# Performance work log

Measured on AMD Instinct MI355X. Metric: run time of the kernel, lower is better.

Reference implementation:

```python
import jax, jax.numpy as jnp
import numpy as np

N = 50000      # nodes
E = 800000     # edges (avg degree 16)
G = 50         # graphs in batch (1000 nodes each)
D_IN, H, H2, OUT = 8, 128, 64, 1


def setup_inputs() -> dict:
    key = jax.random.key(0)
    ks = jax.random.split(key, 16)
    src = jax.random.randint(ks[0], (E,), 0, N)
    # every node gets at least one in-edge (forward computes 3/in_deg)
    dst = jnp.concatenate([jnp.arange(N), jax.random.randint(ks[1], (E - N,), 0, N)])
    graph_ids = jnp.arange(N) // (N // G)

    def lin(k, fan_in, fan_out):
        return jax.random.normal(k, (fan_in, fan_out), jnp.float32) / np.float32(np.sqrt(fan_in))

    inp = {"src": src, "dst": dst, "graph_ids": graph_ids}
    dims = [(D_IN, H), (H, H), (H, H), (H, H), (H, H)]
    for i, (fi, fo) in enumerate(dims):
        inp[f"W{i+1}"] = lin(ks[2 + i], fi, fo)
        inp[f"b{i+1}"] = jnp.zeros((fo,), jnp.float32)
    inp["lw1"] = lin(ks[8], H, H2)
    inp["lb1"] = jnp.zeros((H2,), jnp.float32)
    inp["lw2"] = lin(ks[9], H2, OUT)
    inp["lb2"] = jnp.zeros((OUT,), jnp.float32)
    return inp


def reference(src, dst, graph_ids, W1, b1, W2, b2, W3, b3, W4, b4, W5, b5, lw1, lb1, lw2, lb2):
    ones_e = jnp.ones((E,), jnp.float32)
    in_deg = jax.ops.segment_sum(ones_e, dst, num_segments=N)   # [N]
    out_deg = jax.ops.segment_sum(ones_e, src, num_segments=N)  # [N]

    # degree features (8 channels)
    h1 = in_deg[:, None]
    h2 = (in_deg > 3.0).astype(jnp.float32)[:, None]
    h3 = 3.0 / h1
    h4 = (in_deg > 4.0).astype(jnp.float32)[:, None]
    h_ = jnp.concatenate([h1, h2, h3, h4, -h1, -h2, -h3, -h4], axis=1)  # [N,8]

    # DGL GraphConv norm='both': clamp degrees to min 1 for normalization
    norm_src = jnp.maximum(out_deg, 1.0) ** -0.5  # [N]
    norm_dst = jnp.maximum(in_deg, 1.0) ** -0.5   # [N]

    def conv(h, W, b):
        m = (h * norm_src[:, None])[src]                        # [E, d] gather
        agg = jax.ops.segment_sum(m, dst, num_segments=N)       # [N, d] scatter-add
        return agg * norm_dst[:, None] @ W + b

    h_co = jax.nn.relu(conv(h_, W1, b1))
    h_co = jax.nn.relu(conv(h_co, W2, b2))
    h_co = jax.nn.relu(conv(h_co, W3, b3))
    h_co = jax.nn.relu(conv(h_co, W4, b4))
    h_co = jax.nn.relu(conv(h_co, W5, b5))                      # [N, H]

    # dgl.mean_nodes: per-graph mean pool
    counts = jax.ops.segment_sum(jnp.ones((N,), jnp.float32), graph_ids, num_segments=G)
    graph_emb = jax.ops.segment_sum(h_co, graph_ids, num_segments=G) / counts[:, None]  # [G, H]

    # dropout layers are identity in eval mode
    h_emb = jax.nn.relu(graph_emb @ lw1 + lb1)
    pred = jax.nn.sigmoid(h_emb @ lw2 + lb2)                    # [G, 1]
    return (pred, graph_emb, h_co)
```

## Files before the change

kernel.cpp:

```cpp
#include <hip/hip_runtime.h>
#include <math.h>

#define N_NODES 50000
#define N_EDGES 800000
#define N_GRAPHS 50
#define HD 128
#define TM 64
#define LDA 68
#define POOL_CHUNK 125
#define SCAN_B 256
#define SCAN_NB ((N_NODES + SCAN_B - 1) / SCAN_B)
#define NB_H 128
#define CH_H (N_EDGES / NB_H)
#define NBIN2 (N_NODES / 2)

__global__ __launch_bounds__(256) void k_hist(const int* __restrict__ src,
                                              const int* __restrict__ dst,
                                              unsigned* __restrict__ part_in,
                                              unsigned* __restrict__ part_out) {
    __shared__ unsigned cnt[NBIN2];
    int t = threadIdx.x, b = blockIdx.x;
    int e0 = b * CH_H;
    for (int j = t; j < NBIN2; j += 256) cnt[j] = 0;
    __syncthreads();
    for (int e = e0 + t; e < e0 + CH_H; e += 256) {
        int i = dst[e];
        atomicAdd(&cnt[i >> 1], 1u << ((i & 1) * 16));
    }
    __syncthreads();
    for (int j = t; j < NBIN2; j += 256) part_in[b * NBIN2 + j] = cnt[j];
    __syncthreads();
    for (int j = t; j < NBIN2; j += 256) cnt[j] = 0;
    __syncthreads();
    for (int e = e0 + t; e < e0 + CH_H; e += 256) {
        int i = src[e];
        atomicAdd(&cnt[i >> 1], 1u << ((i & 1) * 16));
    }
    __syncthreads();
    for (int j = t; j < NBIN2; j += 256) part_out[b * NBIN2 + j] = cnt[j];
}

__global__ void k_dreduce(unsigned* __restrict__ part_in,
                          const unsigned* __restrict__ part_out,
                          int* __restrict__ deg_in, int* __restrict__ deg_out) {
    int j = blockIdx.x * blockDim.x + threadIdx.x;
    if (j >= NBIN2) return;
    unsigned run_i = 0, run_o = 0;
    for (int b = 0; b < NB_H; ++b) {
        unsigned pi = part_in[b * NBIN2 + j];
        unsigned po = part_out[b * NBIN2 + j];
        part_in[b * NBIN2 + j] = run_i;
        run_i += pi;
        run_o += po;
    }
    ((int2*)deg_in)[j] = make_int2((int)(run_i & 0xFFFFu), (int)(run_i >> 16));
    ((int2*)deg_out)[j] = make_int2((int)(run_o & 0xFFFFu), (int)(run_o >> 16));
}

__global__ void k_norms(const int* __restrict__ deg_in, const int* __restrict__ deg_out,
                        const int* __restrict__ gids,
                        float* norm_src, float* norm_dst, int* gcount,
                        float4* __restrict__ feat4) {
    __shared__ int hist[N_GRAPHS];
    int t = threadIdx.x;
    if (t < N_GRAPHS) hist[t] = 0;
    __syncthreads();
    int i = blockIdx.x * blockDim.x + t;
    if (i < N_NODES) {
        float di = (float)deg_in[i];
        float dq = (float)deg_out[i];
        float nd = 1.0f / sqrtf(fmaxf(di, 1.0f));
        float ns = 1.0f / sqrtf(fmaxf(dq, 1.0f));
        norm_dst[i] = nd;
        norm_src[i] = ns;
        float4 f;
        f.x = di * ns;
        f.y = (di > 3.0f) ? ns : 0.0f;
        f.z = (3.0f / di) * ns;
        f.w = (di > 4.0f) ? ns : 0.0f;
        feat4[i] = f;
        atomicAdd(&hist[gids[i]], 1);
    }
    __syncthreads();
    if (t < N_GRAPHS && hist[t] != 0) atomicAdd(&gcount[t], hist[t]);
}

__global__ void k_scan1(const int* __restrict__ deg_in, int* off, int* bsum) {
    __shared__ int sh[SCAN_B];
    int t = threadIdx.x;
    int i = blockIdx.x * SCAN_B + t;
    int v = (i < N_NODES) ? deg_in[i] : 0;
    sh[t] = v;
    __syncthreads();
    for (int o = 1; o < SCAN_B; o <<= 1) {
        int u = (t >= o) ? sh[t - o] : 0;
        __syncthreads();
        sh[t] += u;
        __syncthreads();
    }
    if (i < N_NODES) off[i] = sh[t] - v;
    if (t == SCAN_B - 1) bsum[blockIdx.x] = sh[t];
}

__global__ void k_scan2(int* bsum, int* off) {
    __shared__ int sh[SCAN_B];
    int t = threadIdx.x;
    int v = (t < SCAN_NB) ? bsum[t] : 0;
    sh[t] = v;
    __syncthreads();
    for (int o = 1; o < SCAN_B; o <<= 1) {
        int u = (t >= o) ? sh[t - o] : 0;
        __syncthreads();
        sh[t] += u;
        __syncthreads();
    }
    if (t < SCAN_NB) bsum[t] = sh[t] - v;
    if (t == SCAN_B - 1) off[N_NODES] = sh[t];
}

__global__ void k_scan3(int* off, const int* __restrict__ bsum) {
    int b = blockIdx.x, t = threadIdx.x;
    int i = b * SCAN_B + t;
    if (i < N_NODES) off[i] += bsum[b];
}

__global__ __launch_bounds__(256) void k_scatter2(const int* __restrict__ src,
                                                  const int* __restrict__ dst,
                                                  const int* __restrict__ off,
                                                  const unsigned* __restrict__ part_in,
                                                  int* __restrict__ csr) {
    __shared__ unsigned cur[NBIN2];
    int t = threadIdx.x, b = blockIdx.x;
    const unsigned* base = part_in + (size_t)b * NBIN2;
    for (int j = t; j < NBIN2; j += 256) cur[j] = base[j];
    __syncthreads();
    int e0 = b * CH_H;
    for (int e = e0 + t; e < e0 + CH_H; e += 256) {
        int d = dst[e];
        int sh = (d & 1) * 16;
        unsigned old = atomicAdd(&cur[d >> 1], 1u << sh);
        int rank = (int)((old >> sh) & 0xFFFFu);
        csr[off[d] + rank] = src[e];
    }
}

__global__ void k_agg1(const int* __restrict__ off, const int* __restrict__ csr,
                       const float4* __restrict__ feat4,
                       const float* __restrict__ ndst, float* __restrict__ agg8) {
    int i = blockIdx.x * blockDim.x + threadIdx.x;
    if (i >= N_NODES) return;
    int e0 = off[i], e1 = off[i + 1];
    float a0 = 0.f, a1 = 0.f, a2 = 0.f, a3 = 0.f;
    int e = e0;
    for (; e + 1 < e1; e += 2) {
        float4 f0 = feat4[csr[e]];
        float4 f1 = feat4[csr[e + 1]];
        a0 += f0.x + f1.x; a1 += f0.y + f1.y;
        a2 += f0.z + f1.z; a3 += f0.w + f1.w;
    }
    if (e < e1) {
        float4 f0 = feat4[csr[e]];
        a0 += f0.x; a1 += f0.y; a2 += f0.z; a3 += f0.w;
    }
    float nd = ndst[i];
    a0 *= nd; a1 *= nd; a2 *= nd; a3 *= nd;
    float4* p = (float4*)(agg8 + (size_t)i * 8);
    float4 hi = { a0, a1, a2, a3 };
    float4 lo = { -a0, -a1, -a2, -a3 };
    p[0] = hi;
    p[1] = lo;
}

__global__ void k_gemm1(const float* __restrict__ agg8, const float* __restrict__ W,
                        const float* __restrict__ b, const float* __restrict__ nsrc,
                        float* __restrict__ out) {
    __shared__ float Wsh[8 * 128];
    int t = threadIdx.x;
    for (int i = t; i < 1024; i += 256) Wsh[i] = W[i];
    __syncthreads();
    int row = blockIdx.x * 2 + (t >> 7);
    int j = t & 127;
    if (row >= N_NODES) return;
    const float* a = agg8 + (size_t)row * 8;
    float acc = b[j];
#pragma unroll
    for (int k = 0; k < 8; ++k) acc += a[k] * Wsh[k * 128 + j];
    out[(size_t)row * HD + j] = fmaxf(acc, 0.0f) * nsrc[row];
}

__global__ __launch_bounds__(256) void k_agg4(const int* __restrict__ off,
                                              const int* __restrict__ csr,
                                              const float* __restrict__ ndst,
                                              const float* __restrict__ h,
                                              float* __restrict__ out) {
    int wid = (blockIdx.x * blockDim.x + threadIdx.x) >> 6;
    int lane = threadIdx.x & 63;
    if (wid >= N_NODES) return;
    int half = lane >> 5;
    int q = lane & 31;
    int e0 = off[wid], e1 = off[wid + 1];
    float4 a = { 0.f, 0.f, 0.f, 0.f };
    int e = e0 + half;
    for (; e + 6 < e1; e += 8) {
        int s0 = csr[e], s1 = csr[e + 2], s2 = csr[e + 4], s3 = csr[e + 6];
        float4 v0 = *(const float4*)(h + (size_t)s0 * HD + q * 4);
        float4 v1 = *(const float4*)(h + (size_t)s1 * HD + q * 4);
        float4 v2 = *(const float4*)(h + (size_t)s2 * HD + q * 4);
        float4 v3 = *(const float4*)(h + (size_t)s3 * HD + q * 4);
        a.x += v0.x + v1.x + v2.x + v3.x;
        a.y += v0.y + v1.y + v2.y + v3.y;
        a.z += v0.z + v1.z + v2.z + v3.z;
        a.w += v0.w + v1.w + v2.w + v3.w;
    }
    for (; e < e1; e += 2) {
        int s0 = csr[e];
        float4 v0 = *(const float4*)(h + (size_t)s0 * HD + q * 4);
        a.x += v0.x; a.y += v0.y; a.z += v0.z; a.w += v0.w;
    }
    a.x += __shfl_xor(a.x, 32);
    a.y += __shfl_xor(a.y, 32);
    a.z += __shfl_xor(a.z, 32);
    a.w += __shfl_xor(a.w, 32);
    if (half == 0) {
        float nd = ndst[wid];
        a.x *= nd; a.y *= nd; a.z *= nd; a.w *= nd;
        *(float4*)(out + (size_t)wid * HD + q * 4) = a;
    }
}

__global__ void k_agg2(const int* __restrict__ off, const int* __restrict__ csr,
                       const float* __restrict__ ndst,
                       const float* __restrict__ h, float* __restrict__ out) {
    int wid = (blockIdx.x * blockDim.x + threadIdx.x) >> 6;
    int lane = threadIdx.x & 63;
    if (wid >= N_NODES) return;
    int e0 = off[wid], e1 = off[wid + 1];
    float a0 = 0.f, a1 = 0.f;
    int e = e0;
    for (; e + 3 < e1; e += 4) {
        int s0 = csr[e], s1 = csr[e + 1], s2 = csr[e + 2], s3 = csr[e + 3];
        float2 v0 = *(const float2*)(h + (size_t)s0 * HD + lane * 2);
        float2 v1 = *(const float2*)(h + (size_t)s1 * HD + lane * 2);
        float2 v2 = *(const float2*)(h + (size_t)s2 * HD + lane * 2);
        float2 v3 = *(const float2*)(h + (size_t)s3 * HD + lane * 2);
        a0 += v0.x + v1.x + v2.x + v3.x;
        a1 += v0.y + v1.y + v2.y + v3.y;
    }
    for (; e < e1; ++e) {
        int s0 = csr[e];
        float2 v0 = *(const float2*)(h + (size_t)s0 * HD + lane * 2);
        a0 += v0.x; a1 += v0.y;
    }
    float nd = ndst[wid];
    float2 o; o.x = a0 * nd; o.y = a1 * nd;
    *(float2*)(out + (size_t)wid * HD + lane * 2) = o;
}

__global__ __launch_bounds__(512) void k_gemm(const float* __restrict__ A,
                                              const float* __restrict__ W,
                                              const float* __restrict__ b,
                                              const float* __restrict__ nsrc,
                                              int premult,
                                              float* __restrict__ out) {
    __shared__ float Wsh[128 * 128];
    __shared__ float Ash[128 * LDA];
    int t = threadIdx.x;
    const float4* W4 = (const float4*)W;
    float4* Wsh4 = (float4*)Wsh;
#pragma unroll
    for (int i = 0; i < 8; ++i) Wsh4[t + i * 512] = W4[t + i * 512];
    int row0 = blockIdx.x * TM;
#pragma unroll
    for (int i = 0; i < 4; ++i) {
        int idx = t + i * 512;
        int r = idx >> 5;
        int q = idx & 31;
        int row = row0 + r;
        if (row >= N_NODES) row = N_NODES - 1;
        float4 v = ((const float4*)(A + (size_t)row * HD))[q];
        Ash[(4 * q + 0) * LDA + r] = v.x;
        Ash[(4 * q + 1) * LDA + r] = v.y;
        Ash[(4 * q + 2) * LDA + r] = v.z;
        Ash[(4 * q + 3) * LDA + r] = v.w;
    }
    __syncthreads();
    int j0 = (t & 31) * 4;
    int r0 = (t >> 5) * 4;
    float4 bv = *(const float4*)(b + j0);
    float acc[4][4];
#pragma unroll
    for (int r = 0; r < 4; ++r) {
        acc[r][0] = bv.x; acc[r][1] = bv.y; acc[r][2] = bv.z; acc[r][3] = bv.w;
    }
#pragma unroll 4
    for (int k = 0; k < 128; ++k) {
        float4 w = *(const float4*)&Wsh[k * 128 + j0];
        float4 a = *(const float4*)&Ash[k * LDA + r0];
        acc[0][0] += a.x * w.x; acc[0][1] += a.x * w.y; acc[0][2] += a.x * w.z; acc[0][3] += a.x * w.w;
        acc[1][0] += a.y * w.x; acc[1][1] += a.y * w.y; acc[1][2] += a.y * w.z; acc[1][3] += a.y * w.w;
        acc[2][0] += a.z * w.x; acc[2][1] += a.z * w.y; acc[2][2] += a.z * w.z; acc[2][3] += a.z * w.w;
        acc[3][0] += a.w * w.x; acc[3][1] += a.w * w.y; acc[3][2] += a.w * w.z; acc[3][3] += a.w * w.w;
    }
#pragma unroll
    for (int r = 0; r < 4; ++r) {
        int row = row0 + r0 + r;
        if (row < N_NODES) {
            float sc = premult ? nsrc[row] : 1.0f;
            float* op = out + (size_t)row * HD + j0;
            float2 o01 = { fmaxf(acc[r][0], 0.f) * sc, fmaxf(acc[r][1], 0.f) * sc };
            float2 o23 = { fmaxf(acc[r][2], 0.f) * sc, fmaxf(acc[r][3], 0.f) * sc };
            *(float2*)op = o01;
            *(float2*)(op + 2) = o23;
        }
    }
}

__global__ void k_pool(const float* __restrict__ hco, const int* __restrict__ gids,
                       float* gsum) {
    int f = threadIdx.x;
    int n0 = blockIdx.x * POOL_CHUNK;
    int g = gids[n0];
    float s = 0.f;
    for (int i = 0; i < POOL_CHUNK; ++i)
        s += hco[(size_t)(n0 + i) * HD + f];
    atomicAdd(&gsum[g * HD + f], s);
}

__global__ void k_head(const float* __restrict__ gsum, const int* __restrict__ gcount,
                       const float* __restrict__ lw1, const float* __restrict__ lb1,
                       const float* __restrict__ lw2, const float* __restrict__ lb2,
                       float* __restrict__ dout) {
    __shared__ float ge[128];
    int g = blockIdx.x, j = threadIdx.x;
    float cnt = (float)gcount[g];
    float g0 = gsum[g * HD + j] / cnt;
    float g1 = gsum[g * HD + 64 + j] / cnt;
    ge[j] = g0; ge[64 + j] = g1;
    dout[N_GRAPHS + g * HD + j] = g0;
    dout[N_GRAPHS + g * HD + 64 + j] = g1;
    __syncthreads();
    float acc = lb1[j];
#pragma unroll 4
    for (int k = 0; k < 128; ++k) acc += ge[k] * lw1[k * 64 + j];
    float he = fmaxf(acc, 0.f);
    float p = he * lw2[j];
#pragma unroll
    for (int o = 32; o > 0; o >>= 1) p += __shfl_down(p, o);
    if (j == 0) dout[g] = 1.0f / (1.0f + expf(-(p + lb2[0])));
}

extern "C" void kernel_launch(void* const* d_in, const int* in_sizes, int n_in,
                              void* d_out, int out_size, void* d_ws, size_t ws_size,
                              hipStream_t stream) {
    const int* src  = (const int*)d_in[0];
    const int* dst  = (const int*)d_in[1];
    const int* gids = (const int*)d_in[2];
    const float* W1 = (const float*)d_in[3];  const float* b1 = (const float*)d_in[4];
    const float* W2 = (const float*)d_in[5];  const float* b2 = (const float*)d_in[6];
    const float* W3 = (const float*)d_in[7];  const float* b3 = (const float*)d_in[8];
    const float* W4 = (const float*)d_in[9];  const float* b4 = (const float*)d_in[10];
    const float* W5 = (const float*)d_in[11]; const float* b5 = (const float*)d_in[12];
    const float* lw1 = (const float*)d_in[13]; const float* lb1 = (const float*)d_in[14];
    const float* lw2 = (const float*)d_in[15]; const float* lb2 = (const float*)d_in[16];
    float* out = (float*)d_out;

    char* ws = (char*)d_ws;
    int*    gcount   = (int*)(ws + 0);
    float*  gsum     = (float*)(ws + 256);
    const size_t ZERO_BYTES = 25856;
    int*    deg_in   = (int*)(ws + 26112);
    int*    deg_out  = (int*)(ws + 226304);
    int*    off      = (int*)(ws + 426496);
    int*    csr      = (int*)(ws + 826880);
    float*  norm_src = (float*)(ws + 4026880);
    float*  norm_dst = (float*)(ws + 4227072);
    int*    bsum     = (int*)(ws + 4427264);
    float4* feat4    = (float4*)(ws + 4428288);
    float*  aggbuf   = (float*)(ws + 5228544);
    float*  hws      = (float*)(ws + 30828544);
    const size_t WS_NEEDED = 30828544 + 25600000;

    unsigned* part_in  = (unsigned*)aggbuf;
    unsigned* part_out = (unsigned*)aggbuf + NB_H * NBIN2;

    float* hco = out + (N_GRAPHS + N_GRAPHS * HD);
    bool aligned = (ws_size >= WS_NEEDED);
    float* hbuf = aligned ? hws : hco;

    hipMemsetAsync(ws, 0, ZERO_BYTES, stream);

    k_hist<<<NB_H, 256, 0, stream>>>(src, dst, part_in, part_out);
    k_dreduce<<<(NBIN2 + 255) / 256, 256, 0, stream>>>(part_in, part_out,
                                                       deg_in, deg_out);
    k_norms<<<(N_NODES + 255) / 256, 256, 0, stream>>>(deg_in, deg_out, gids,
                                                       norm_src, norm_dst, gcount, feat4);
    k_scan1<<<SCAN_NB, SCAN_B, 0, stream>>>(deg_in, off, bsum);
    k_scan2<<<1, SCAN_B, 0, stream>>>(bsum, off);
    k_scan3<<<SCAN_NB, SCAN_B, 0, stream>>>(off, bsum);
    k_scatter2<<<NB_H, 256, 0, stream>>>(src, dst, off, part_in, csr);

    k_agg1<<<(N_NODES + 255) / 256, 256, 0, stream>>>(off, csr, feat4, norm_dst, aggbuf);
    k_gemm1<<<N_NODES / 2, 256, 0, stream>>>(aggbuf, W1, b1, norm_src, hbuf);

    const float* Ws[4] = { W2, W3, W4, W5 };
    const float* bs[4] = { b2, b3, b4, b5 };
    for (int L = 0; L < 4; ++L) {
        if (aligned)
            k_agg4<<<(N_NODES * 64 + 255) / 256, 256, 0, stream>>>(off, csr,
                                                                   norm_dst, hbuf, aggbuf);
        else
            k_agg2<<<(N_NODES * 64 + 255) / 256, 256, 0, stream>>>(off, csr,
                                                                   norm_dst, hbuf, aggbuf);
        float* gout = (L < 3) ? hbuf : hco;
        k_gemm<<<(N_NODES + TM - 1) / TM, 512, 0, stream>>>(aggbuf, Ws[L], bs[L],
                                                            norm_src, (L < 3) ? 1 : 0,
                                                            gout);
    }

    k_pool<<<N_NODES / POOL_CHUNK, 128, 0, stream>>>(hco, gids, gsum);
    k_head<<<N_GRAPHS, 64, 0, stream>>>(gsum, gcount, lw1, lb1, lw2, lb2, out);
}
```

Measured before the change: 519.7 us.

## Store hidden features in 16-column strips and retile the dense GEMM

Hidden features are written in a column-strip layout (8 strips of 16 floats per node), so each aggregation pass gathers 64-byte rows from a 3.2MB strip that fits in cache. This is meant to cut the random-gather DRAM traffic of the 128-wide aggregation. The GEMM moves from 64-row tiles with 4x4 per-thread blocks to 128-row tiles with 8x8 per-thread blocks and a padded, swizzled shared layout. The larger tiles need more LDS and registers per thread, which may lower occupancy, and the aggregation kernel now runs 8 times as many blocks.

```diff
diff --git a/kernel.cpp b/kernel.cpp
--- a/kernel.cpp
+++ b/kernel.cpp
@@ -5,14 +5,20 @@
 #define N_EDGES 800000
 #define N_GRAPHS 50
 #define HD 128
-#define TM 64
-#define LDA 68
 #define POOL_CHUNK 125
 #define SCAN_B 256
 #define SCAN_NB ((N_NODES + SCAN_B - 1) / SCAN_B)
 #define NB_H 128
 #define CH_H (N_EDGES / NB_H)
 #define NBIN2 (N_NODES / 2)
+#define NPASS 8
+#define STRIP 16
+#define NPBLK (N_NODES / 4)
+#define GLDA 140
+
+__device__ __forceinline__ int sidx(int k, int c) {
+    return k * GLDA + c + ((c >> 5) << 2);
+}
 
 __global__ __launch_bounds__(256) void k_hist(const int* __restrict__ src,
                                               const int* __restrict__ dst,
@@ -173,7 +179,7 @@
 
 __global__ void k_gemm1(const float* __restrict__ agg8, const float* __restrict__ W,
                         const float* __restrict__ b, const float* __restrict__ nsrc,
-                        float* __restrict__ out) {
+                        int blocked, float* __restrict__ out) {
     __shared__ float Wsh[8 * 128];
     int t = threadIdx.x;
     for (int i = t; i < 1024; i += 256) Wsh[i] = W[i];
@@ -185,46 +191,42 @@
     float acc = b[j];
 #pragma unroll
     for (int k = 0; k < 8; ++k) acc += a[k] * Wsh[k * 128 + j];
-    out[(size_t)row * HD + j] = fmaxf(acc, 0.0f) * nsrc[row];
-}
-
-__global__ __launch_bounds__(256) void k_agg4(const int* __restrict__ off,
+    float v = fmaxf(acc, 0.0f) * nsrc[row];
+    if (blocked)
+        out[((size_t)(j >> 4) * N_NODES + row) * STRIP + (j & 15)] = v;
+    else
+        out[(size_t)row * HD + j] = v;
+}
+
+__global__ __launch_bounds__(256) void k_aggp(const int* __restrict__ off,
                                               const int* __restrict__ csr,
                                               const float* __restrict__ ndst,
                                               const float* __restrict__ h,
-                                              float* __restrict__ out) {
-    int wid = (blockIdx.x * blockDim.x + threadIdx.x) >> 6;
+                                              float* __restrict__ agg) {
+    int bx = blockIdx.x;
+    int pass = bx / NPBLK;
+    int node = (bx - pass * NPBLK) * 4 + (threadIdx.x >> 6);
     int lane = threadIdx.x & 63;
-    if (wid >= N_NODES) return;
-    int half = lane >> 5;
-    int q = lane & 31;
-    int e0 = off[wid], e1 = off[wid + 1];
+    int slot = lane >> 2, q = lane & 3;
+    const float* hp = h + (size_t)pass * N_NODES * STRIP;
+    int e0 = off[node], e1 = off[node + 1];
     float4 a = { 0.f, 0.f, 0.f, 0.f };
-    int e = e0 + half;
-    for (; e + 6 < e1; e += 8) {
-        int s0 = csr[e], s1 = csr[e + 2], s2 = csr[e + 4], s3 = csr[e + 6];
-        float4 v0 = *(const float4*)(h + (size_t)s0 * HD + q * 4);
-        float4 v1 = *(const float4*)(h + (size_t)s1 * HD + q * 4);
-        float4 v2 = *(const float4*)(h + (size_t)s2 * HD + q * 4);
-        float4 v3 = *(const float4*)(h + (size_t)s3 * HD + q * 4);
-        a.x += v0.x + v1.x + v2.x + v3.x;
-        a.y += v0.y + v1.y + v2.y + v3.y;
-        a.z += v0.z + v1.z + v2.z + v3.z;
-        a.w += v0.w + v1.w + v2.w + v3.w;
-    }
-    for (; e < e1; e += 2) {
-        int s0 = csr[e];
-        float4 v0 = *(const float4*)(h + (size_t)s0 * HD + q * 4);
-        a.x += v0.x; a.y += v0.y; a.z += v0.z; a.w += v0.w;
-    }
-    a.x += __shfl_xor(a.x, 32);
-    a.y += __shfl_xor(a.y, 32);
-    a.z += __shfl_xor(a.z, 32);
-    a.w += __shfl_xor(a.w, 32);
-    if (half == 0) {
-        float nd = ndst[wid];
-        a.x *= nd; a.y *= nd; a.z *= nd; a.w *= nd;
-        *(float4*)(out + (size_t)wid * HD + q * 4) = a;
+    for (int e = e0 + slot; e < e1; e += 16) {
+        int s = csr[e];
+        float4 v = *(const float4*)(hp + (size_t)s * STRIP + q * 4);
+        a.x += v.x; a.y += v.y; a.z += v.z; a.w += v.w;
+    }
+#pragma unroll
+    for (int m = 4; m <= 32; m <<= 1) {
+        a.x += __shfl_xor(a.x, m);
+        a.y += __shfl_xor(a.y, m);
+        a.z += __shfl_xor(a.z, m);
+        a.w += __shfl_xor(a.w, m);
+    }
+    if (lane < 4) {
+        float nd = ndst[node];
+        float4 o = { a.x * nd, a.y * nd, a.z * nd, a.w * nd };
+        *(float4*)(agg + (size_t)node * HD + pass * STRIP + lane * 4) = o;
     }
 }
 
@@ -256,61 +258,88 @@
     *(float2*)(out + (size_t)wid * HD + lane * 2) = o;
 }
 
-__global__ __launch_bounds__(512) void k_gemm(const float* __restrict__ A,
+__global__ __launch_bounds__(256) void k_gemm(const float* __restrict__ A,
                                               const float* __restrict__ W,
                                               const float* __restrict__ b,
                                               const float* __restrict__ nsrc,
-                                              int premult,
+                                              int mode,
                                               float* __restrict__ out) {
-    __shared__ float Wsh[128 * 128];
-    __shared__ float Ash[128 * LDA];
+    __shared__ float Wsh[128 * GLDA];
+    __shared__ float Ash[128 * GLDA];
     int t = threadIdx.x;
-    const float4* W4 = (const float4*)W;
-    float4* Wsh4 = (float4*)Wsh;
-#pragma unroll
-    for (int i = 0; i < 8; ++i) Wsh4[t + i * 512] = W4[t + i * 512];
-    int row0 = blockIdx.x * TM;
-#pragma unroll
-    for (int i = 0; i < 4; ++i) {
-        int idx = t + i * 512;
-        int r = idx >> 5;
-        int q = idx & 31;
-        int row = row0 + r;
-        if (row >= N_NODES) row = N_NODES - 1;
-        float4 v = ((const float4*)(A + (size_t)row * HD))[q];
-        Ash[(4 * q + 0) * LDA + r] = v.x;
-        Ash[(4 * q + 1) * LDA + r] = v.y;
-        Ash[(4 * q + 2) * LDA + r] = v.z;
-        Ash[(4 * q + 3) * LDA + r] = v.w;
-    }
-    __syncthreads();
-    int j0 = (t & 31) * 4;
-    int r0 = (t >> 5) * 4;
-    float4 bv = *(const float4*)(b + j0);
-    float acc[4][4];
-#pragma unroll
-    for (int r = 0; r < 4; ++r) {
-        acc[r][0] = bv.x; acc[r][1] = bv.y; acc[r][2] = bv.z; acc[r][3] = bv.w;
-    }
-#pragma unroll 4
+    int row0 = blockIdx.x * 128;
+    {
+        const float4* W4 = (const float4*)W;
+#pragma unroll
+        for (int i = 0; i < 16; ++i) {
+            int idx = t + i * 256;
+            int k = idx >> 5;
+            int q = idx & 31;
+            float4 v = W4[idx];
+            Wsh[sidx(k, 4 * q + 0)] = v.x;
+            Wsh[sidx(k, 4 * q + 1)] = v.y;
+            Wsh[sidx(k, 4 * q + 2)] = v.z;
+            Wsh[sidx(k, 4 * q + 3)] = v.w;
+        }
+        const float4* A4 = (const float4*)A;
+#pragma unroll
+        for (int i = 0; i < 16; ++i) {
+            int idx = t + i * 256;
+            int q = idx >> 7;
+            int r = idx & 127;
+            int row = row0 + r;
+            if (row >= N_NODES) row = N_NODES - 1;
+            float4 v = A4[(size_t)row * 32 + q];
+            Ash[sidx(4 * q + 0, r)] = v.x;
+            Ash[sidx(4 * q + 1, r)] = v.y;
+            Ash[sidx(4 * q + 2, r)] = v.z;
+            Ash[sidx(4 * q + 3, r)] = v.w;
+        }
+    }
+    __syncthreads();
+    int tx = t & 15, ty = t >> 4;
+    int j0 = tx * 8, r0 = ty * 8;
+    float acc[8][8];
+#pragma unroll
+    for (int c = 0; c < 8; ++c) {
+        float bc = b[j0 + c];
+#pragma unroll
+        for (int r = 0; r < 8; ++r) acc[r][c] = bc;
+    }
+#pragma unroll 2
     for (int k = 0; k < 128; ++k) {
-        float4 w = *(const float4*)&Wsh[k * 128 + j0];
-        float4 a = *(const float4*)&Ash[k * LDA + r0];
-        acc[0][0] += a.x * w.x; acc[0][1] += a.x * w.y; acc[0][2] += a.x * w.z; acc[0][3] += a.x * w.w;
-        acc[1][0] += a.y * w.x; acc[1][1] += a.y * w.y; acc[1][2] += a.y * w.z; acc[1][3] += a.y * w.w;
-        acc[2][0] += a.z * w.x; acc[2][1] += a.z * w.y; acc[2][2] += a.z * w.z; acc[2][3] += a.z * w.w;
-        acc[3][0] += a.w * w.x; acc[3][1] += a.w * w.y; acc[3][2] += a.w * w.z; acc[3][3] += a.w * w.w;
-    }
-#pragma unroll
-    for (int r = 0; r < 4; ++r) {
+        float4 w0 = *(const float4*)&Wsh[sidx(k, j0)];
+        float4 w1 = *(const float4*)&Wsh[sidx(k, j0 + 4)];
+        float4 a0 = *(const float4*)&Ash[sidx(k, r0)];
+        float4 a1 = *(const float4*)&Ash[sidx(k, r0 + 4)];
+        float wv[8] = { w0.x, w0.y, w0.z, w0.w, w1.x, w1.y, w1.z, w1.w };
+        float av[8] = { a0.x, a0.y, a0.z, a0.w, a1.x, a1.y, a1.z, a1.w };
+#pragma unroll
+        for (int r = 0; r < 8; ++r)
+#pragma unroll
+            for (int c = 0; c < 8; ++c) acc[r][c] += av[r] * wv[c];
+    }
+#pragma unroll
+    for (int r = 0; r < 8; ++r) {
         int row = row0 + r0 + r;
-        if (row < N_NODES) {
-            float sc = premult ? nsrc[row] : 1.0f;
+        if (row >= N_NODES) continue;
+        if (mode == 0) {
+            float sc = nsrc[row];
+            float* op = out + ((size_t)(j0 >> 4) * N_NODES + row) * STRIP + (j0 & 15);
+            float4 o0 = { fmaxf(acc[r][0], 0.f) * sc, fmaxf(acc[r][1], 0.f) * sc,
+                          fmaxf(acc[r][2], 0.f) * sc, fmaxf(acc[r][3], 0.f) * sc };
+            float4 o1 = { fmaxf(acc[r][4], 0.f) * sc, fmaxf(acc[r][5], 0.f) * sc,
+                          fmaxf(acc[r][6], 0.f) * sc, fmaxf(acc[r][7], 0.f) * sc };
+            *(float4*)op = o0;
+            *(float4*)(op + 4) = o1;
+        } else {
+            float sc = (mode == 1) ? nsrc[row] : 1.0f;
             float* op = out + (size_t)row * HD + j0;
-            float2 o01 = { fmaxf(acc[r][0], 0.f) * sc, fmaxf(acc[r][1], 0.f) * sc };
-            float2 o23 = { fmaxf(acc[r][2], 0.f) * sc, fmaxf(acc[r][3], 0.f) * sc };
-            *(float2*)op = o01;
-            *(float2*)(op + 2) = o23;
+#pragma unroll
+            for (int c = 0; c < 8; c += 2) {
+                float2 o = { fmaxf(acc[r][c], 0.f) * sc, fmaxf(acc[r][c + 1], 0.f) * sc };
+                *(float2*)(op + c) = o;
+            }
         }
     }
 }
@@ -385,7 +414,6 @@
 
     float* hco = out + (N_GRAPHS + N_GRAPHS * HD);
     bool aligned = (ws_size >= WS_NEEDED);
-    float* hbuf = aligned ? hws : hco;
 
     hipMemsetAsync(ws, 0, ZERO_BYTES, stream);
 
@@ -400,21 +428,22 @@
     k_scatter2<<<NB_H, 256, 0, stream>>>(src, dst, off, part_in, csr);
 
     k_agg1<<<(N_NODES + 255) / 256, 256, 0, stream>>>(off, csr, feat4, norm_dst, aggbuf);
-    k_gemm1<<<N_NODES / 2, 256, 0, stream>>>(aggbuf, W1, b1, norm_src, hbuf);
+    float* hbuf = aligned ? hws : hco;
+    k_gemm1<<<N_NODES / 2, 256, 0, stream>>>(aggbuf, W1, b1, norm_src,
+                                             aligned ? 1 : 0, hbuf);
 
     const float* Ws[4] = { W2, W3, W4, W5 };
     const float* bs[4] = { b2, b3, b4, b5 };
     for (int L = 0; L < 4; ++L) {
         if (aligned)
-            k_agg4<<<(N_NODES * 64 + 255) / 256, 256, 0, stream>>>(off, csr,
-                                                                   norm_dst, hbuf, aggbuf);
+            k_aggp<<<NPASS * NPBLK, 256, 0, stream>>>(off, csr, norm_dst, hws, aggbuf);
         else
             k_agg2<<<(N_NODES * 64 + 255) / 256, 256, 0, stream>>>(off, csr,
-                                                                   norm_dst, hbuf, aggbuf);
+                                                                   norm_dst, hco, aggbuf);
+        int mode = (L < 3) ? (aligned ? 0 : 1) : 2;
         float* gout = (L < 3) ? hbuf : hco;
-        k_gemm<<<(N_NODES + TM - 1) / TM, 512, 0, stream>>>(aggbuf, Ws[L], bs[L],
-                                                            norm_src, (L < 3) ? 1 : 0,
-                                                            gout);
+        k_gemm<<<(N_NODES + 127) / 128, 256, 0, stream>>>(aggbuf, Ws[L], bs[L],
+                                                          norm_src, mode, gout);
     }
 
     k_pool<<<N_NODES / POOL_CHUNK, 128, 0, stream>>>(hco, gids, gsum);
```

After: 769.1 us. 1.48x slower.

## Fuse neighbor aggregation into GEMM kernel for hidden GCN layers

Applied to the files above, without the earlier changes.

Replaces the separate aggregation and GEMM launches of layers 2-5 with one kernel. Each 512-thread block gathers and sums neighbor features for its 64 nodes straight into shared memory, then multiplies by the weight tile held in shared memory. Layer outputs ping-pong between two buffers. This removes the round trip of the aggregated matrix through global memory and half the launches. In exchange, each block now runs a serial gather of 8 nodes per wavefront before its GEMM, with heavy shared-memory use limiting occupancy, so latency hiding in the gather may get worse. The fallback GEMM load is also split into two float2 loads, apparently for alignment.

```diff
diff --git a/kernel.cpp b/kernel.cpp
--- a/kernel.cpp
+++ b/kernel.cpp
@@ -188,43 +188,91 @@
     out[(size_t)row * HD + j] = fmaxf(acc, 0.0f) * nsrc[row];
 }
 
-__global__ __launch_bounds__(256) void k_agg4(const int* __restrict__ off,
-                                              const int* __restrict__ csr,
-                                              const float* __restrict__ ndst,
-                                              const float* __restrict__ h,
-                                              float* __restrict__ out) {
-    int wid = (blockIdx.x * blockDim.x + threadIdx.x) >> 6;
-    int lane = threadIdx.x & 63;
-    if (wid >= N_NODES) return;
-    int half = lane >> 5;
-    int q = lane & 31;
-    int e0 = off[wid], e1 = off[wid + 1];
-    float4 a = { 0.f, 0.f, 0.f, 0.f };
-    int e = e0 + half;
-    for (; e + 6 < e1; e += 8) {
-        int s0 = csr[e], s1 = csr[e + 2], s2 = csr[e + 4], s3 = csr[e + 6];
-        float4 v0 = *(const float4*)(h + (size_t)s0 * HD + q * 4);
-        float4 v1 = *(const float4*)(h + (size_t)s1 * HD + q * 4);
-        float4 v2 = *(const float4*)(h + (size_t)s2 * HD + q * 4);
-        float4 v3 = *(const float4*)(h + (size_t)s3 * HD + q * 4);
-        a.x += v0.x + v1.x + v2.x + v3.x;
-        a.y += v0.y + v1.y + v2.y + v3.y;
-        a.z += v0.z + v1.z + v2.z + v3.z;
-        a.w += v0.w + v1.w + v2.w + v3.w;
-    }
-    for (; e < e1; e += 2) {
-        int s0 = csr[e];
-        float4 v0 = *(const float4*)(h + (size_t)s0 * HD + q * 4);
-        a.x += v0.x; a.y += v0.y; a.z += v0.z; a.w += v0.w;
-    }
-    a.x += __shfl_xor(a.x, 32);
-    a.y += __shfl_xor(a.y, 32);
-    a.z += __shfl_xor(a.z, 32);
-    a.w += __shfl_xor(a.w, 32);
-    if (half == 0) {
-        float nd = ndst[wid];
-        a.x *= nd; a.y *= nd; a.z *= nd; a.w *= nd;
-        *(float4*)(out + (size_t)wid * HD + q * 4) = a;
+__global__ __launch_bounds__(512) void k_aggemm(const int* __restrict__ off,
+                                                const int* __restrict__ csr,
+                                                const float* __restrict__ ndst,
+                                                const float* __restrict__ h,
+                                                const float* __restrict__ W,
+                                                const float* __restrict__ b,
+                                                const float* __restrict__ nsrc,
+                                                int premult,
+                                                float* __restrict__ out) {
+    __shared__ float Wsh[128 * 128];
+    __shared__ float Ash[128 * LDA];
+    int t = threadIdx.x;
+    const float4* W4 = (const float4*)W;
+    float4* Wsh4 = (float4*)Wsh;
+#pragma unroll
+    for (int i = 0; i < 8; ++i) Wsh4[t + i * 512] = W4[t + i * 512];
+
+    int row0 = blockIdx.x * TM;
+    int w = t >> 6, lane = t & 63;
+    int half = lane >> 5, q = lane & 31;
+    for (int i = 0; i < 8; ++i) {
+        int r = w * 8 + i;
+        int node = row0 + r;
+        if (node >= N_NODES) break;
+        int e0 = off[node], e1 = off[node + 1];
+        float4 a = { 0.f, 0.f, 0.f, 0.f };
+        int e = e0 + half;
+        for (; e + 6 < e1; e += 8) {
+            int s0 = csr[e], s1 = csr[e + 2], s2 = csr[e + 4], s3 = csr[e + 6];
+            float4 v0 = *(const float4*)(h + (size_t)s0 * HD + q * 4);
+            float4 v1 = *(const float4*)(h + (size_t)s1 * HD + q * 4);
+            float4 v2 = *(const float4*)(h + (size_t)s2 * HD + q * 4);
+            float4 v3 = *(const float4*)(h + (size_t)s3 * HD + q * 4);
+            a.x += v0.x + v1.x + v2.x + v3.x;
+            a.y += v0.y + v1.y + v2.y + v3.y;
+            a.z += v0.z + v1.z + v2.z + v3.z;
+            a.w += v0.w + v1.w + v2.w + v3.w;
+        }
+        for (; e < e1; e += 2) {
+            int s0 = csr[e];
+            float4 v0 = *(const float4*)(h + (size_t)s0 * HD + q * 4);
+            a.x += v0.x; a.y += v0.y; a.z += v0.z; a.w += v0.w;
+        }
+        a.x += __shfl_xor(a.x, 32);
+        a.y += __shfl_xor(a.y, 32);
+        a.z += __shfl_xor(a.z, 32);
+        a.w += __shfl_xor(a.w, 32);
+        if (half == 0) {
+            float nd = ndst[node];
+            Ash[(4 * q + 0) * LDA + r] = a.x * nd;
+            Ash[(4 * q + 1) * LDA + r] = a.y * nd;
+            Ash[(4 * q + 2) * LDA + r] = a.z * nd;
+            Ash[(4 * q + 3) * LDA + r] = a.w * nd;
+        }
+    }
+    __syncthreads();
+
+    int j0 = (t & 31) * 4;
+    int r0 = (t >> 5) * 4;
+    float4 bv = *(const float4*)(b + j0);
+    float acc[4][4];
+#pragma unroll
+    for (int r = 0; r < 4; ++r) {
+        acc[r][0] = bv.x; acc[r][1] = bv.y; acc[r][2] = bv.z; acc[r][3] = bv.w;
+    }
+#pragma unroll 4
+    for (int k = 0; k < 128; ++k) {
+        float4 wv = *(const float4*)&Wsh[k * 128 + j0];
+        float4 av = *(const float4*)&Ash[k * LDA + r0];
+        acc[0][0] += av.x * wv.x; acc[0][1] += av.x * wv.y; acc[0][2] += av.x * wv.z; acc[0][3] += av.x * wv.w;
+        acc[1][0] += av.y * wv.x; acc[1][1] += av.y * wv.y; acc[1][2] += av.y * wv.z; acc[1][3] += av.y * wv.w;
+        acc[2][0] += av.z * wv.x; acc[2][1] += av.z * wv.y; acc[2][2] += av.z * wv.z; acc[2][3] += av.z * wv.w;
+        acc[3][0] += av.w * wv.x; acc[3][1] += av.w * wv.y; acc[3][2] += av.w * wv.z; acc[3][3] += av.w * wv.w;
+    }
+#pragma unroll
+    for (int r = 0; r < 4; ++r) {
+        int row = row0 + r0 + r;
+        if (row < N_NODES) {
+            float sc = premult ? nsrc[row] : 1.0f;
+            float* op = out + (size_t)row * HD + j0;
+            float2 o01 = { fmaxf(acc[r][0], 0.f) * sc, fmaxf(acc[r][1], 0.f) * sc };
+            float2 o23 = { fmaxf(acc[r][2], 0.f) * sc, fmaxf(acc[r][3], 0.f) * sc };
+            *(float2*)op = o01;
+            *(float2*)(op + 2) = o23;
+        }
     }
 }
 
@@ -277,11 +325,13 @@
         int q = idx & 31;
         int row = row0 + r;
         if (row >= N_NODES) row = N_NODES - 1;
-        float4 v = ((const float4*)(A + (size_t)row * HD))[q];
-        Ash[(4 * q + 0) * LDA + r] = v.x;
-        Ash[(4 * q + 1) * LDA + r] = v.y;
-        Ash[(4 * q + 2) * LDA + r] = v.z;
-        Ash[(4 * q + 3) * LDA + r] = v.w;
+        const float* ap = A + (size_t)row * HD + q * 4;
+        float2 vlo = *(const float2*)ap;
+        float2 vhi = *(const float2*)(ap + 2);
+        Ash[(4 * q + 0) * LDA + r] = vlo.x;
+        Ash[(4 * q + 1) * LDA + r] = vlo.y;
+        Ash[(4 * q + 2) * LDA + r] = vhi.x;
+        Ash[(4 * q + 3) * LDA + r] = vhi.y;
     }
     __syncthreads();
     int j0 = (t & 31) * 4;
@@ -294,12 +344,12 @@
     }
 #pragma unroll 4
     for (int k = 0; k < 128; ++k) {
-        float4 w = *(const float4*)&Wsh[k * 128 + j0];
-        float4 a = *(const float4*)&Ash[k * LDA + r0];
-        acc[0][0] += a.x * w.x; acc[0][1] += a.x * w.y; acc[0][2] += a.x * w.z; acc[0][3] += a.x * w.w;
-        acc[1][0] += a.y * w.x; acc[1][1] += a.y * w.y; acc[1][2] += a.y * w.z; acc[1][3] += a.y * w.w;
-        acc[2][0] += a.z * w.x; acc[2][1] += a.z * w.y; acc[2][2] += a.z * w.z; acc[2][3] += a.z * w.w;
-        acc[3][0] += a.w * w.x; acc[3][1] += a.w * w.y; acc[3][2] += a.w * w.z; acc[3][3] += a.w * w.w;
+        float4 wv = *(const float4*)&Wsh[k * 128 + j0];
+        float4 av = *(const float4*)&Ash[k * LDA + r0];
+        acc[0][0] += av.x * wv.x; acc[0][1] += av.x * wv.y; acc[0][2] += av.x * wv.z; acc[0][3] += av.x * wv.w;
+        acc[1][0] += av.y * wv.x; acc[1][1] += av.y * wv.y; acc[1][2] += av.y * wv.z; acc[1][3] += av.y * wv.w;
+        acc[2][0] += av.z * wv.x; acc[2][1] += av.z * wv.y; acc[2][2] += av.z * wv.z; acc[2][3] += av.z * wv.w;
+        acc[3][0] += av.w * wv.x; acc[3][1] += av.w * wv.y; acc[3][2] += av.w * wv.z; acc[3][3] += av.w * wv.w;
     }
 #pragma unroll
     for (int r = 0; r < 4; ++r) {
@@ -385,7 +435,6 @@
 
     float* hco = out + (N_GRAPHS + N_GRAPHS * HD);
     bool aligned = (ws_size >= WS_NEEDED);
-    float* hbuf = aligned ? hws : hco;
 
     hipMemsetAsync(ws, 0, ZERO_BYTES, stream);
 
@@ -399,22 +448,27 @@
     k_scan3<<<SCAN_NB, SCAN_B, 0, stream>>>(off, bsum);
     k_scatter2<<<NB_H, 256, 0, stream>>>(src, dst, off, part_in, csr);
 
+    float* hA = aligned ? hws : hco;
     k_agg1<<<(N_NODES + 255) / 256, 256, 0, stream>>>(off, csr, feat4, norm_dst, aggbuf);
-    k_gemm1<<<N_NODES / 2, 256, 0, stream>>>(aggbuf, W1, b1, norm_src, hbuf);
+    k_gemm1<<<N_NODES / 2, 256, 0, stream>>>(aggbuf, W1, b1, norm_src, hA);
 
     const float* Ws[4] = { W2, W3, W4, W5 };
     const float* bs[4] = { b2, b3, b4, b5 };
     for (int L = 0; L < 4; ++L) {
-        if (aligned)
-            k_agg4<<<(N_NODES * 64 + 255) / 256, 256, 0, stream>>>(off, csr,
-                                                                   norm_dst, hbuf, aggbuf);
-        else
+        int premult = (L < 3) ? 1 : 0;
+        if (aligned) {
+            const float* hin = (L & 1) ? aggbuf : hws;
+            float* gout = (L < 3) ? ((L & 1) ? hws : aggbuf) : hco;
+            k_aggemm<<<(N_NODES + TM - 1) / TM, 512, 0, stream>>>(off, csr, norm_dst,
+                                                                  hin, Ws[L], bs[L],
+                                                                  norm_src, premult, gout);
+        } else {
+            float* gout = (L < 3) ? hco : hco;
             k_agg2<<<(N_NODES * 64 + 255) / 256, 256, 0, stream>>>(off, csr,
-                                                                   norm_dst, hbuf, aggbuf);
-        float* gout = (L < 3) ? hbuf : hco;
-        k_gemm<<<(N_NODES + TM - 1) / TM, 512, 0, stream>>>(aggbuf, Ws[L], bs[L],
-                                                            norm_src, (L < 3) ? 1 : 0,
-                                                            gout);
+                                                                   norm_dst, hco, aggbuf);
+            k_gemm<<<(N_NODES + TM - 1) / TM, 512, 0, stream>>>(aggbuf, Ws[L], bs[L],
+                                                                norm_src, premult, gout);
+        }
     }
 
     k_pool<<<N_NODES / POOL_CHUNK, 128, 0, stream>>>(hco, gids, gsum);
```

After: 662.6 us. 27.5% more time.

## Split GEMM output columns across two blocks and store A row-major with padding

Applied to the files above, without the earlier changes.

The dense 128x128 layer GEMM is retiled so each 256-thread block computes a 64-row by 64-column output tile, with a 2D grid covering both column halves. This halves the per-block W staging and shared memory use to raise occupancy. The A tile is now kept row-major with stride 129 instead of transposed, which avoids the strided transpose stores but turns the inner loop's A reads into four scalar LDS loads. The trade-off is that each A row is loaded from global memory twice, once per column half.

```diff
diff --git a/kernel.cpp b/kernel.cpp
--- a/kernel.cpp
+++ b/kernel.cpp
@@ -6,13 +6,13 @@
 #define N_GRAPHS 50
 #define HD 128
 #define TM 64
-#define LDA 68
 #define POOL_CHUNK 125
 #define SCAN_B 256
 #define SCAN_NB ((N_NODES + SCAN_B - 1) / SCAN_B)
 #define NB_H 128
 #define CH_H (N_EDGES / NB_H)
 #define NBIN2 (N_NODES / 2)
+#define ALDA 129
 
 __global__ __launch_bounds__(256) void k_hist(const int* __restrict__ src,
                                               const int* __restrict__ dst,
@@ -256,37 +256,41 @@
     *(float2*)(out + (size_t)wid * HD + lane * 2) = o;
 }
 
-__global__ __launch_bounds__(512) void k_gemm(const float* __restrict__ A,
-                                              const float* __restrict__ W,
-                                              const float* __restrict__ b,
-                                              const float* __restrict__ nsrc,
-                                              int premult,
-                                              float* __restrict__ out) {
-    __shared__ float Wsh[128 * 128];
-    __shared__ float Ash[128 * LDA];
+__global__ __launch_bounds__(256) void k_gemm2(const float* __restrict__ A,
+                                               const float* __restrict__ W,
+                                               const float* __restrict__ b,
+                                               const float* __restrict__ nsrc,
+                                               int premult,
+                                               float* __restrict__ out) {
+    __shared__ float Wsh[128 * 64];
+    __shared__ float Ash[64 * ALDA];
     int t = threadIdx.x;
+    int row0 = blockIdx.x * TM;
+    int jh = blockIdx.y * 64;
     const float4* W4 = (const float4*)W;
-    float4* Wsh4 = (float4*)Wsh;
-#pragma unroll
-    for (int i = 0; i < 8; ++i) Wsh4[t + i * 512] = W4[t + i * 512];
-    int row0 = blockIdx.x * TM;
-#pragma unroll
-    for (int i = 0; i < 4; ++i) {
-        int idx = t + i * 512;
+#pragma unroll
+    for (int i = 0; i < 8; ++i) {
+        int idx = t + i * 256;
+        int k = idx >> 4;
+        int q = idx & 15;
+        ((float4*)Wsh)[k * 16 + q] = W4[k * 32 + (jh >> 2) + q];
+    }
+    const float4* A4 = (const float4*)A;
+#pragma unroll
+    for (int i = 0; i < 8; ++i) {
+        int idx = t + i * 256;
         int r = idx >> 5;
         int q = idx & 31;
         int row = row0 + r;
         if (row >= N_NODES) row = N_NODES - 1;
-        float4 v = ((const float4*)(A + (size_t)row * HD))[q];
-        Ash[(4 * q + 0) * LDA + r] = v.x;
-        Ash[(4 * q + 1) * LDA + r] = v.y;
-        Ash[(4 * q + 2) * LDA + r] = v.z;
-        Ash[(4 * q + 3) * LDA + r] = v.w;
-    }
-    __syncthreads();
-    int j0 = (t & 31) * 4;
-    int r0 = (t >> 5) * 4;
-    float4 bv = *(const float4*)(b + j0);
+        float4 v = A4[(size_t)row * 32 + q];
+        float* ap = &Ash[r * ALDA + 4 * q];
+        ap[0] = v.x; ap[1] = v.y; ap[2] = v.z; ap[3] = v.w;
+    }
+    __syncthreads();
+    int jq = (t & 15) * 4;
+    int r0 = (t >> 4) * 4;
+    float4 bv = *(const float4*)(b + jh + jq);
     float acc[4][4];
 #pragma unroll
     for (int r = 0; r < 4; ++r) {
@@ -294,19 +298,22 @@
     }
 #pragma unroll 4
     for (int k = 0; k < 128; ++k) {
-        float4 w = *(const float4*)&Wsh[k * 128 + j0];
-        float4 a = *(const float4*)&Ash[k * LDA + r0];
-        acc[0][0] += a.x * w.x; acc[0][1] += a.x * w.y; acc[0][2] += a.x * w.z; acc[0][3] += a.x * w.w;
-        acc[1][0] += a.y * w.x; acc[1][1] += a.y * w.y; acc[1][2] += a.y * w.z; acc[1][3] += a.y * w.w;
-        acc[2][0] += a.z * w.x; acc[2][1] += a.z * w.y; acc[2][2] += a.z * w.z; acc[2][3] += a.z * w.w;
-        acc[3][0] += a.w * w.x; acc[3][1] += a.w * w.y; acc[3][2] += a.w * w.z; acc[3][3] += a.w * w.w;
+        float4 wv = *(const float4*)&Wsh[k * 64 + jq];
+        float a0 = Ash[(r0 + 0) * ALDA + k];
+        float a1 = Ash[(r0 + 1) * ALDA + k];
+        float a2 = Ash[(r0 + 2) * ALDA + k];
+        float a3 = Ash[(r0 + 3) * ALDA + k];
+        acc[0][0] += a0 * wv.x; acc[0][1] += a0 * wv.y; acc[0][2] += a0 * wv.z; acc[0][3] += a0 * wv.w;
+        acc[1][0] += a1 * wv.x; acc[1][1] += a1 * wv.y; acc[1][2] += a1 * wv.z; acc[1][3] += a1 * wv.w;
+        acc[2][0] += a2 * wv.x; acc[2][1] += a2 * wv.y; acc[2][2] += a2 * wv.z; acc[2][3] += a2 * wv.w;
+        acc[3][0] += a3 * wv.x; acc[3][1] += a3 * wv.y; acc[3][2] += a3 * wv.z; acc[3][3] += a3 * wv.w;
     }
 #pragma unroll
     for (int r = 0; r < 4; ++r) {
         int row = row0 + r0 + r;
         if (row < N_NODES) {
             float sc = premult ? nsrc[row] : 1.0f;
-            float* op = out + (size_t)row * HD + j0;
+            float* op = out + (size_t)row * HD + jh + jq;
             float2 o01 = { fmaxf(acc[r][0], 0.f) * sc, fmaxf(acc[r][1], 0.f) * sc };
             float2 o23 = { fmaxf(acc[r][2], 0.f) * sc, fmaxf(acc[r][3], 0.f) * sc };
             *(float2*)op = o01;
@@ -404,6 +411,7 @@
 
     const float* Ws[4] = { W2, W3, W4, W5 };
     const float* bs[4] = { b2, b3, b4, b5 };
+    dim3 ggrid((N_NODES + TM - 1) / TM, 2);
     for (int L = 0; L < 4; ++L) {
         if (aligned)
             k_agg4<<<(N_NODES * 64 + 255) / 256, 256, 0, stream>>>(off, csr,
@@ -412,9 +420,8 @@
             k_agg2<<<(N_NODES * 64 + 255) / 256, 256, 0, stream>>>(off, csr,
                                                                    norm_dst, hbuf, aggbuf);
         float* gout = (L < 3) ? hbuf : hco;
-        k_gemm<<<(N_NODES + TM - 1) / TM, 512, 0, stream>>>(aggbuf, Ws[L], bs[L],
-                                                            norm_src, (L < 3) ? 1 : 0,
-                                                            gout);
+        k_gemm2<<<ggrid, 256, 0, stream>>>(aggbuf, Ws[L], bs[L],
+                                           norm_src, (L < 3) ? 1 : 0, gout);
     }
 
     k_pool<<<N_NODES / POOL_CHUNK, 128, 0, stream>>>(hco, gids, gsum);
```

Measured after the change: 487.3 us. 1.07x faster.
